# Kernel tuning notes

Hardware: AMD Instinct MI355X
Metric: run time of the kernel (lower is better)

The kernel has to match this reference:

```python
import jax, jax.numpy as jnp
import numpy as np

B, S, H = 1024, 512, 768
NUM_CLASSES = 3


def setup_inputs() -> dict:
    key = jax.random.key(0)
    k1, k2, k3, k4 = jax.random.split(key, 4)
    embeddings = jax.random.normal(k1, (B, S, H), dtype=jnp.float32)
    # labels 0..4; 2/3/4 mark pronoun, entity A, entity B tokens
    mentions = jax.random.randint(k2, (B, S), 0, 5, dtype=jnp.int64)
    W1 = jax.random.normal(k3, (3 * H, 512), dtype=jnp.float32) * 0.02
    b1 = jnp.zeros((512,), dtype=jnp.float32)
    W2 = jax.random.normal(k4, (512, NUM_CLASSES), dtype=jnp.float32) * 0.02
    b2 = jnp.zeros((NUM_CLASSES,), dtype=jnp.float32)
    return {"embeddings": embeddings, "mentions": mentions,
            "W1": W1, "b1": b1, "W2": W2, "b2": b2}


def _masked_mean(embeddings, mentions, label):
    # embeddings: [B,S,H], mentions: [B,S] -> [B,H]
    mask = (mentions == label).astype(embeddings.dtype)  # [B,S]
    s = jnp.einsum('bsh,bs->bh', embeddings, mask)
    c = jnp.sum(mask, axis=1, keepdims=True)             # [B,1]
    return s / c


def reference(embeddings, mentions, W1, b1, W2, b2):
    # Dropout is identity in eval mode. Vectorized replacement of the
    # python loop + growing torch.cat: three segment-mean pools, concat,
    # then 2-layer MLP classifier.
    pronouns = _masked_mean(embeddings, mentions, 2)
    entities_a = _masked_mean(embeddings, mentions, 3)
    entities_b = _masked_mean(embeddings, mentions, 4)
    o = jnp.concatenate([pronouns, entities_a, entities_b], axis=-1)  # [B,3H]
    h = jax.nn.relu(o @ W1 + b1)
    return h @ W2 + b2
```

## Files before the change

kernel.cpp:

```cpp
#include <hip/hip_runtime.h>
#include <hip/hip_bf16.h>

#define B_SZ 1024
#define S_SZ 512
#define H_SZ 768
#define K3H  2304
#define HID  512
#define NC   3

typedef __attribute__((ext_vector_type(8)))  __bf16        bf16x8;
typedef __attribute__((ext_vector_type(16))) float         f32x16;
typedef __attribute__((ext_vector_type(8)))  unsigned short ushort8x;

__device__ __forceinline__ unsigned short f2bf(float f) {
    unsigned u = __builtin_bit_cast(unsigned, f);
    unsigned r = (u + 0x7fffu + ((u >> 16) & 1u)) >> 16;
    return (unsigned short)r;
}

__global__ __launch_bounds__(192) void pool_kernel(
        const float* __restrict__ emb,
        const int*   __restrict__ men,
        unsigned short* __restrict__ o)
{
    const int b = blockIdx.x;
    const int t = threadIdx.x;

    __shared__ unsigned short sel[S_SZ];
    __shared__ int nsel_sh;
    __shared__ int cnt[3];

    if (t < 64) {
        int basep = 0;
        int c0 = 0, c1 = 0, c2 = 0;
        #pragma unroll
        for (int ch = 0; ch < 8; ++ch) {
            int s = ch * 64 + t;
            int m = men[(size_t)b * S_SZ + s];
            bool pick = (m >= 2);
            unsigned long long mk = __ballot(pick);
            int pos = basep + __popcll(mk & ((1ull << t) - 1ull));
            if (pick) sel[pos] = (unsigned short)(s | ((m - 2) << 12));
            basep += __popcll(mk);
            c0 += (m == 2);
            c1 += (m == 3);
            c2 += (m == 4);
        }
        #pragma unroll
        for (int off = 32; off > 0; off >>= 1) {
            c0 += __shfl_down(c0, off);
            c1 += __shfl_down(c1, off);
            c2 += __shfl_down(c2, off);
        }
        if (t == 0) { nsel_sh = basep; cnt[0] = c0; cnt[1] = c1; cnt[2] = c2; }
    }
    __syncthreads();

    const int ns = nsel_sh;
    float4 a0 = {0.f,0.f,0.f,0.f}, a1 = {0.f,0.f,0.f,0.f}, a2 = {0.f,0.f,0.f,0.f};
    const float4* base =
        reinterpret_cast<const float4*>(emb + (size_t)b * S_SZ * H_SZ);

    #define ACCUM(E, V) do {                                             \
        int tg_ = (E) >> 12;                                             \
        if (tg_ == 0)      { a0.x+=V.x; a0.y+=V.y; a0.z+=V.z; a0.w+=V.w; } \
        else if (tg_ == 1) { a1.x+=V.x; a1.y+=V.y; a1.z+=V.z; a1.w+=V.w; } \
        else               { a2.x+=V.x; a2.y+=V.y; a2.z+=V.z; a2.w+=V.w; } \
    } while (0)

    int i = 0;
    for (; i + 4 <= ns; i += 4) {
        int e0 = sel[i], e1 = sel[i+1], e2 = sel[i+2], e3 = sel[i+3];
        float4 v0 = base[(e0 & 0x1ff) * 192 + t];
        float4 v1 = base[(e1 & 0x1ff) * 192 + t];
        float4 v2 = base[(e2 & 0x1ff) * 192 + t];
        float4 v3 = base[(e3 & 0x1ff) * 192 + t];
        ACCUM(e0, v0); ACCUM(e1, v1); ACCUM(e2, v2); ACCUM(e3, v3);
    }
    for (; i < ns; ++i) {
        int e = sel[i];
        float4 v = base[(e & 0x1ff) * 192 + t];
        ACCUM(e, v);
    }
    #undef ACCUM

    const float r0 = 1.f / (float)cnt[0];
    const float r1 = 1.f / (float)cnt[1];
    const float r2 = 1.f / (float)cnt[2];

    unsigned short* op = o + (size_t)b * K3H;
    ushort4 w0 = { f2bf(a0.x*r0), f2bf(a0.y*r0), f2bf(a0.z*r0), f2bf(a0.w*r0) };
    ushort4 w1 = { f2bf(a1.x*r1), f2bf(a1.y*r1), f2bf(a1.z*r1), f2bf(a1.w*r1) };
    ushort4 w2 = { f2bf(a2.x*r2), f2bf(a2.y*r2), f2bf(a2.z*r2), f2bf(a2.w*r2) };
    *reinterpret_cast<ushort4*>(op + 0 * H_SZ + t * 4) = w0;
    *reinterpret_cast<ushort4*>(op + 1 * H_SZ + t * 4) = w1;
    *reinterpret_cast<ushort4*>(op + 2 * H_SZ + t * 4) = w2;
}

__global__ __launch_bounds__(256) void transpose_kernel(
        const float* __restrict__ W1, unsigned short* __restrict__ Bt)
{
    __shared__ unsigned short tile[32][33];
    const int kb = blockIdx.x * 32, nb = blockIdx.y * 32;
    const int c = threadIdx.x & 31, r0 = threadIdx.x >> 5;
    #pragma unroll
    for (int i = 0; i < 4; ++i) {
        int r = r0 + i * 8;
        tile[r][c] = f2bf(W1[(size_t)(kb + r) * HID + nb + c]);
    }
    __syncthreads();
    #pragma unroll
    for (int i = 0; i < 4; ++i) {
        int r = r0 + i * 8;
        Bt[(size_t)(nb + r) * K3H + kb + c] = tile[c][r];
    }
}

__global__ __launch_bounds__(256) void mlp1_kernel(
        const unsigned short* __restrict__ A,
        const unsigned short* __restrict__ Bt,
        const float* __restrict__ bias,
        float*       __restrict__ C)
{
    __shared__ unsigned short As[64][72];
    __shared__ unsigned short Bs[64][72];

    const int t  = threadIdx.x;
    const int m0 = blockIdx.y * 64;
    const int n0 = blockIdx.x * 64;
    const int w  = t >> 6, l = t & 63;
    const int wr = w >> 1, wc = w & 1;
    const int lr = l & 31;
    const int lk = (l >> 5) * 8;
    const int sr = t >> 3;
    const int sk = (t & 7) * 8;

    f32x16 acc = {0.f,0.f,0.f,0.f,0.f,0.f,0.f,0.f,
                  0.f,0.f,0.f,0.f,0.f,0.f,0.f,0.f};

    for (int k0 = 0; k0 < K3H; k0 += 64) {
        __syncthreads();
        ushort8x ga0 = *(const ushort8x*)&A [(size_t)(m0 + sr     ) * K3H + k0 + sk];
        ushort8x ga1 = *(const ushort8x*)&A [(size_t)(m0 + sr + 32) * K3H + k0 + sk];
        ushort8x gb0 = *(const ushort8x*)&Bt[(size_t)(n0 + sr     ) * K3H + k0 + sk];
        ushort8x gb1 = *(const ushort8x*)&Bt[(size_t)(n0 + sr + 32) * K3H + k0 + sk];
        *(ushort8x*)&As[sr     ][sk] = ga0;
        *(ushort8x*)&As[sr + 32][sk] = ga1;
        *(ushort8x*)&Bs[sr     ][sk] = gb0;
        *(ushort8x*)&Bs[sr + 32][sk] = gb1;
        __syncthreads();

        #pragma unroll
        for (int kk = 0; kk < 64; kk += 16) {
            bf16x8 af = *(const bf16x8*)&As[wr * 32 + lr][kk + lk];
            bf16x8 bf = *(const bf16x8*)&Bs[wc * 32 + lr][kk + lk];
            acc = __builtin_amdgcn_mfma_f32_32x32x16_bf16(af, bf, acc, 0, 0, 0);
        }
    }

    const int col = n0 + wc * 32 + lr;
    const float bv = bias[col];
    #pragma unroll
    for (int r = 0; r < 16; ++r) {
        int row = (r & 3) + 8 * (r >> 2) + 4 * (l >> 5);
        float v = acc[r] + bv;
        C[(size_t)(m0 + wr * 32 + row) * HID + col] = fmaxf(v, 0.f);
    }
}

__global__ __launch_bounds__(64) void mlp2_kernel(
        const float* __restrict__ h,
        const float* __restrict__ W2,
        const float* __restrict__ b2,
        float*       __restrict__ out)
{
    const int b = blockIdx.x;
    const int l = threadIdx.x;
    float a0 = 0.f, a1 = 0.f, a2 = 0.f;
    for (int k = l; k < HID; k += 64) {
        float hv = h[(size_t)b * HID + k];
        a0 += hv * W2[k * 3 + 0];
        a1 += hv * W2[k * 3 + 1];
        a2 += hv * W2[k * 3 + 2];
    }
    #pragma unroll
    for (int off = 32; off > 0; off >>= 1) {
        a0 += __shfl_down(a0, off);
        a1 += __shfl_down(a1, off);
        a2 += __shfl_down(a2, off);
    }
    if (l == 0) {
        out[b * 3 + 0] = a0 + b2[0];
        out[b * 3 + 1] = a1 + b2[1];
        out[b * 3 + 2] = a2 + b2[2];
    }
}

extern "C" void kernel_launch(void* const* d_in, const int* in_sizes, int n_in,
                              void* d_out, int out_size, void* d_ws, size_t ws_size,
                              hipStream_t stream) {
    const float* emb = (const float*)d_in[0];
    const int*   men = (const int*)  d_in[1];
    const float* W1  = (const float*)d_in[2];
    const float* b1  = (const float*)d_in[3];
    const float* W2  = (const float*)d_in[4];
    const float* b2  = (const float*)d_in[5];
    float* out = (float*)d_out;

    unsigned short* o_bf = (unsigned short*)d_ws;
    unsigned short* w1t  = o_bf + (size_t)B_SZ * K3H;
    float*          h    = (float*)(w1t + (size_t)HID * K3H);

    transpose_kernel<<<dim3(K3H / 32, HID / 32), 256, 0, stream>>>(W1, w1t);
    pool_kernel<<<B_SZ, 192, 0, stream>>>(emb, men, o_bf);
    mlp1_kernel<<<dim3(HID / 64, B_SZ / 64), 256, 0, stream>>>(o_bf, w1t, b1, h);
    mlp2_kernel<<<B_SZ, 64, 0, stream>>>(h, W2, b2, out);
}
```

Measured before the change: 218.5 us.

## Double-buffer LDS with register prefetch and XOR swizzle in MLP1 GEMM

Restructures the MLP1 bf16 MFMA GEMM so the next K tile is loaded from global memory into registers while MFMAs run on the current LDS buffer, then stored into a second LDS buffer. LDS layout switches from padded rows to an XOR-swizzled layout to avoid bank conflicts on fragment reads. This hides global load latency but doubles LDS use, adds register pressure, and keeps two barriers per step.

```diff
diff --git a/kernel.cpp b/kernel.cpp
--- a/kernel.cpp
+++ b/kernel.cpp
@@ -122,8 +122,7 @@
         const float* __restrict__ bias,
         float*       __restrict__ C)
 {
-    __shared__ unsigned short As[64][72];
-    __shared__ unsigned short Bs[64][72];
+    __shared__ unsigned short lds[2][2][64 * 64];
 
     const int t  = threadIdx.x;
     const int m0 = blockIdx.y * 64;
@@ -131,30 +130,67 @@
     const int w  = t >> 6, l = t & 63;
     const int wr = w >> 1, wc = w & 1;
     const int lr = l & 31;
-    const int lk = (l >> 5) * 8;
-    const int sr = t >> 3;
-    const int sk = (t & 7) * 8;
+    const int hi = l >> 5;
+    const int sw = lr & 7;
+
+    const int s_row0 = t >> 3;
+    const int s_row1 = 32 + (t >> 3);
+    const int s_slot = t & 7;
+
+    const unsigned short* a_p0 = A  + (size_t)(m0 + s_row0) * K3H + s_slot * 8;
+    const unsigned short* a_p1 = A  + (size_t)(m0 + s_row1) * K3H + s_slot * 8;
+    const unsigned short* b_p0 = Bt + (size_t)(n0 + s_row0) * K3H + s_slot * 8;
+    const unsigned short* b_p1 = Bt + (size_t)(n0 + s_row1) * K3H + s_slot * 8;
+
+    const int w_idx0 = s_row0 * 64 + ((s_slot ^ (s_row0 & 7)) * 8);
+    const int w_idx1 = s_row1 * 64 + ((s_slot ^ (s_row1 & 7)) * 8);
 
     f32x16 acc = {0.f,0.f,0.f,0.f,0.f,0.f,0.f,0.f,
                   0.f,0.f,0.f,0.f,0.f,0.f,0.f,0.f};
 
-    for (int k0 = 0; k0 < K3H; k0 += 64) {
-        __syncthreads();
-        ushort8x ga0 = *(const ushort8x*)&A [(size_t)(m0 + sr     ) * K3H + k0 + sk];
-        ushort8x ga1 = *(const ushort8x*)&A [(size_t)(m0 + sr + 32) * K3H + k0 + sk];
-        ushort8x gb0 = *(const ushort8x*)&Bt[(size_t)(n0 + sr     ) * K3H + k0 + sk];
-        ushort8x gb1 = *(const ushort8x*)&Bt[(size_t)(n0 + sr + 32) * K3H + k0 + sk];
-        *(ushort8x*)&As[sr     ][sk] = ga0;
-        *(ushort8x*)&As[sr + 32][sk] = ga1;
-        *(ushort8x*)&Bs[sr     ][sk] = gb0;
-        *(ushort8x*)&Bs[sr + 32][sk] = gb1;
-        __syncthreads();
-
+    ushort8x ra0 = *(const ushort8x*)(a_p0);
+    ushort8x ra1 = *(const ushort8x*)(a_p1);
+    ushort8x rb0 = *(const ushort8x*)(b_p0);
+    ushort8x rb1 = *(const ushort8x*)(b_p1);
+    *(ushort8x*)&lds[0][0][w_idx0] = ra0;
+    *(ushort8x*)&lds[0][0][w_idx1] = ra1;
+    *(ushort8x*)&lds[0][1][w_idx0] = rb0;
+    *(ushort8x*)&lds[0][1][w_idx1] = rb1;
+    __syncthreads();
+
+    const int NT = K3H / 64;
+    int cur = 0;
+    const int a_frag_row = (wr * 32 + lr) * 64;
+    const int b_frag_row = (wc * 32 + lr) * 64;
+
+    for (int step = 0; step < NT; ++step) {
+        if (step + 1 < NT) {
+            const size_t koff = (size_t)(step + 1) * 64;
+            ra0 = *(const ushort8x*)(a_p0 + koff);
+            ra1 = *(const ushort8x*)(a_p1 + koff);
+            rb0 = *(const ushort8x*)(b_p0 + koff);
+            rb1 = *(const ushort8x*)(b_p1 + koff);
+        }
+
+        const unsigned short* As = lds[cur][0];
+        const unsigned short* Bs = lds[cur][1];
         #pragma unroll
         for (int kk = 0; kk < 64; kk += 16) {
-            bf16x8 af = *(const bf16x8*)&As[wr * 32 + lr][kk + lk];
-            bf16x8 bf = *(const bf16x8*)&Bs[wc * 32 + lr][kk + lk];
+            const int ks = (kk >> 3) + hi;
+            bf16x8 af = *(const bf16x8*)&As[a_frag_row + ((ks ^ sw) * 8)];
+            bf16x8 bf = *(const bf16x8*)&Bs[b_frag_row + ((ks ^ sw) * 8)];
             acc = __builtin_amdgcn_mfma_f32_32x32x16_bf16(af, bf, acc, 0, 0, 0);
+        }
+        __syncthreads();
+
+        if (step + 1 < NT) {
+            const int nb = cur ^ 1;
+            *(ushort8x*)&lds[nb][0][w_idx0] = ra0;
+            *(ushort8x*)&lds[nb][0][w_idx1] = ra1;
+            *(ushort8x*)&lds[nb][1][w_idx0] = rb0;
+            *(ushort8x*)&lds[nb][1][w_idx1] = rb1;
+            __syncthreads();
+            cur = nb;
         }
     }
 
@@ -162,7 +198,7 @@
     const float bv = bias[col];
     #pragma unroll
     for (int r = 0; r < 16; ++r) {
-        int row = (r & 3) + 8 * (r >> 2) + 4 * (l >> 5);
+        int row = (r & 3) + 8 * (r >> 2) + 4 * hi;
         float v = acc[r] + bv;
         C[(size_t)(m0 + wr * 32 + row) * HID + col] = fmaxf(v, 0.f);
     }
```

After: 215.0 us. No clear change (-1.6%).
